# Kernel optimization log

Hardware: AMD Instinct MI355X
Metric: run time of the kernel (lower is better)

Reference implementation:

```python
import jax, jax.numpy as jnp
import numpy as np

N_GRAPHS = 1000  # static number of segments for mean pooling
NUM_STEPS = 6


def setup_inputs() -> dict:
    key = jax.random.key(0)
    ks = jax.random.split(key, 20)
    N, E, G = 100000, 1600000, N_GRAPHS
    H, FN, FE = 64, 9, 3

    def init(k, shape, fan_in):
        return (jax.random.normal(k, shape) / np.sqrt(fan_in)).astype(jnp.float32)

    return {
        "x": jax.random.normal(ks[0], (N, FN), dtype=jnp.float32),
        "edge_index": jax.random.randint(ks[1], (2, E), 0, N, dtype=jnp.int32),
        "edge_attr": jax.random.normal(ks[2], (E, FE), dtype=jnp.float32),
        "batch": jnp.sort(jax.random.randint(ks[3], (N,), 0, G, dtype=jnp.int32)),
        # message MLP: Linear(FN+FE -> H), ReLU, Linear(H -> H)
        "msg_W1": init(ks[4], (H, FN + FE), FN + FE), "msg_b1": jnp.zeros((H,), jnp.float32),
        "msg_W2": init(ks[5], (H, H), H), "msg_b2": jnp.zeros((H,), jnp.float32),
        # GRUCell(H, H): torch layout weight_ih [3H, H], weight_hh [3H, H]
        "gru_Wih": init(ks[6], (3 * H, H), H), "gru_Whh": init(ks[7], (3 * H, H), H),
        "gru_bih": jnp.zeros((3 * H,), jnp.float32), "gru_bhh": jnp.zeros((3 * H,), jnp.float32),
        # readout: Linear(H -> H), ReLU, Dropout(eval: identity), Linear(H -> 1)
        "read_W1": init(ks[8], (H, H), H), "read_b1": jnp.zeros((H,), jnp.float32),
        "read_W2": init(ks[9], (1, H), H), "read_b2": jnp.zeros((1,), jnp.float32),
    }


def reference(x, edge_index, edge_attr, batch,
              msg_W1, msg_b1, msg_W2, msg_b2,
              gru_Wih, gru_Whh, gru_bih, gru_bhh,
              read_W1, read_b1, read_W2, read_b2):
    N = x.shape[0]
    H = msg_W2.shape[0]
    src, dst = edge_index[0], edge_index[1]

    # Messages depend only on x[src] and edge_attr, which never change across
    # steps, so (identically to the torch loop) compute them once.
    m_in = jnp.concatenate([x[src], edge_attr], axis=1)          # [E, FN+FE]
    h1 = jax.nn.relu(m_in @ msg_W1.T + msg_b1)                    # [E, H]
    messages = h1 @ msg_W2.T + msg_b2                             # [E, H]
    aggregated = jax.ops.segment_sum(messages, dst, num_segments=N)  # [N, H]

    # GRU input-gate projections of `aggregated` are also step-invariant.
    gi = aggregated @ gru_Wih.T + gru_bih                          # [N, 3H]
    i_r, i_z, i_n = jnp.split(gi, 3, axis=1)

    h = jnp.zeros((N, H), dtype=x.dtype)
    for _ in range(NUM_STEPS):
        gh = h @ gru_Whh.T + gru_bhh                               # [N, 3H]
        h_r, h_z, h_n = jnp.split(gh, 3, axis=1)
        r = jax.nn.sigmoid(i_r + h_r)
        z = jax.nn.sigmoid(i_z + h_z)
        n = jnp.tanh(i_n + r * h_n)
        h = (1.0 - z) * n + z * h

    # global_mean_pool
    sums = jax.ops.segment_sum(h, batch, num_segments=N_GRAPHS)    # [G, H]
    counts = jax.ops.segment_sum(jnp.ones((N,), h.dtype), batch, num_segments=N_GRAPHS)
    pooled = sums / jnp.maximum(counts, 1.0)[:, None]

    out = jax.nn.relu(pooled @ read_W1.T + read_b1)                # dropout=eval identity
    return out @ read_W2.T + read_b2                               # [G, 1]
```

## Files before the change

kernel.cpp:

```cpp
#include <hip/hip_runtime.h>
#include <math.h>

#define CH 1024
#define LOG2E 1.4426950408889634f

typedef __attribute__((ext_vector_type(8))) short bf16x8;
typedef __attribute__((ext_vector_type(4))) float f32x4;
typedef __attribute__((ext_vector_type(4))) unsigned u32x4;

__device__ __forceinline__ float rcp_(float x){ return __builtin_amdgcn_rcpf(x); }
__device__ __forceinline__ float exp2_(float x){ return exp2f(x); }
__device__ __forceinline__ unsigned short f2bf(float f){
  union{float f;unsigned u;}v; v.f=f;
  unsigned r = v.u + 0x7fffu + ((v.u>>16)&1u);
  return (unsigned short)(r>>16);
}
__device__ __forceinline__ float bf2f(unsigned short u){
  union{unsigned u; float f;} v; v.u = ((unsigned)u) << 16; return v.f;
}

__global__ __launch_bounds__(256) void count_rank(const int* __restrict__ ei, int* __restrict__ cnt,
                                                  int* __restrict__ rank, int E){
  int e = blockIdx.x*256 + threadIdx.x;
  if (e < E) rank[e] = atomicAdd(&cnt[ei[E + e]], 1);
}

__global__ __launch_bounds__(256) void scan_partial(const int* __restrict__ cnt, int* __restrict__ bsum, int N){
  __shared__ int s[256];
  int b = blockIdx.x, t = threadIdx.x;
  int base = b*CH;
  int sum = 0;
  for (int i = t; i < CH; i += 256){ int idx = base + i; sum += (idx < N) ? cnt[idx] : 0; }
  s[t] = sum; __syncthreads();
  for (int off = 128; off > 0; off >>= 1){ if (t < off) s[t] += s[t+off]; __syncthreads(); }
  if (t == 0) bsum[b] = s[0];
}

__global__ void scan_bsum(int* __restrict__ bsum, int B){
  if (threadIdx.x == 0 && blockIdx.x == 0){
    int acc = 0;
    for (int i = 0; i < B; i++){ int v = bsum[i]; bsum[i] = acc; acc += v; }
  }
}

__global__ __launch_bounds__(256) void scan_final(const int* __restrict__ cnt, const int* __restrict__ bsum,
                                                  int* __restrict__ off, float* __restrict__ degf, int N, int E){
  __shared__ int s[256];
  __shared__ int sx[256];
  int b = blockIdx.x, t = threadIdx.x;
  int i0 = b*CH + t*4;
  int v0 = (i0   < N) ? cnt[i0]   : 0;
  int v1 = (i0+1 < N) ? cnt[i0+1] : 0;
  int v2 = (i0+2 < N) ? cnt[i0+2] : 0;
  int v3 = (i0+3 < N) ? cnt[i0+3] : 0;
  s[t] = v0+v1+v2+v3; __syncthreads();
  if (t == 0){ int acc = bsum[b]; for (int i = 0; i < 256; i++){ sx[i] = acc; acc += s[i]; } }
  __syncthreads();
  int acc = sx[t];
  if (i0   < N){ off[i0]   = acc; degf[i0]   = (float)v0; } acc += v0;
  if (i0+1 < N){ off[i0+1] = acc; degf[i0+1] = (float)v1; } acc += v1;
  if (i0+2 < N){ off[i0+2] = acc; degf[i0+2] = (float)v2; } acc += v2;
  if (i0+3 < N){ off[i0+3] = acc; degf[i0+3] = (float)v3; }
  if (b == 0 && t == 0) off[N] = E;
}

__global__ __launch_bounds__(256) void xpack_kernel(const float* __restrict__ x, unsigned short* __restrict__ xp, int N){
  int n = blockIdx.x*256 + threadIdx.x;
  if (n >= N) return;
  const float* xr = x + (size_t)n*9;
  union { unsigned short us[32]; u32x4 q[4]; } row;
  #pragma unroll
  for (int i = 0; i < 9; i++){
    unsigned short hi = f2bf(xr[i]);
    unsigned short lo = f2bf(xr[i] - bf2f(hi));
    if (i < 8){ row.us[i] = hi; row.us[8+i] = lo; }
    else { row.us[16] = hi; row.us[17] = lo; }
  }
  #pragma unroll
  for (int i = 18; i < 32; i++) row.us[i] = 0;
  u32x4* dstp = (u32x4*)(xp + (size_t)n*32);
  dstp[0] = row.q[0]; dstp[1] = row.q[1]; dstp[2] = row.q[2]; dstp[3] = row.q[3];
}

__global__ __launch_bounds__(256) void fill64(const int* __restrict__ ei, const unsigned short* __restrict__ xp,
                                              const float* __restrict__ ea, const int* __restrict__ off,
                                              const int* __restrict__ rank, float* __restrict__ csr2, int E){
  int e = blockIdx.x*256 + threadIdx.x;
  if (e >= E) return;
  int dst = ei[E + e];
  int src = ei[e];
  int p = off[dst] + rank[e];
  const u32x4* xr4 = (const u32x4*)(xp + (size_t)src*32);
  u32x4 q0 = xr4[0];
  u32x4 q1 = xr4[1];
  unsigned hl8 = *(const unsigned*)(xp + (size_t)src*32 + 16);
  const float* er = ea + (size_t)e*3;
  float e0 = er[0], e1 = er[1], e2 = er[2];
  unsigned short eh0 = f2bf(e0), eh1 = f2bf(e1), eh2 = f2bf(e2);
  unsigned short el0 = f2bf(e0 - bf2f(eh0));
  unsigned short el1 = f2bf(e1 - bf2f(eh1));
  unsigned short el2 = f2bf(e2 - bf2f(eh2));
  u32x4 q2;
  q2.x = (hl8 & 0xFFFFu) | ((unsigned)eh0 << 16);
  q2.y = (unsigned)eh1 | ((unsigned)eh2 << 16);
  q2.z = (hl8 >> 16)    | ((unsigned)el0 << 16);
  q2.w = (unsigned)el1 | ((unsigned)el2 << 16);
  u32x4 q3 = {0u, 0u, 0u, 0u};
  u32x4* row = (u32x4*)(csr2 + (size_t)p*16);
  row[0] = q0; row[1] = q1; row[2] = q2; row[3] = q3;
}

__global__ __launch_bounds__(256) void pack_frag(const float* __restrict__ W, unsigned short* __restrict__ P,
                                                 float sRZ, float sN){
  int o = blockIdx.x*256 + threadIdx.x;
  if (o >= 12288) return;
  int j = o & 7, l = (o>>3)&63, kh = (o>>9)&1, c = o>>10;
  float sc = (c < 8) ? sRZ : sN;
  P[o] = f2bf(sc * W[(c*16 + (l&15))*64 + kh*32 + 8*(l>>4) + j]);
}

__global__ __launch_bounds__(256) void pack_w1(const float* __restrict__ W1,
    unsigned short* __restrict__ B1, unsigned short* __restrict__ B2){
  int o = blockIdx.x*256 + threadIdx.x;
  if (o >= 2048) return;
  int j = o & 7, l = (o>>3) & 63, c = o >> 9;
  int n = c*16 + (l & 15);
  int kk = 8*(l>>4) + j;
  unsigned short b1v = 0, b2v = 0;
  if (kk < 12){
    float w = W1[n*12 + kk];
    unsigned short hi = f2bf(w);
    b1v = hi;
    b2v = f2bf(w - bf2f(hi));
  } else if (kk >= 16 && kk < 28){
    b1v = f2bf(W1[n*12 + (kk-16)]);
  }
  B1[o] = b1v; B2[o] = b2v;
}

__global__ __launch_bounds__(256) void make_M(const float* __restrict__ Wih, const float* __restrict__ W2,
    const float* __restrict__ b2, float* __restrict__ M, float* __restrict__ dv){
  int idx = blockIdx.x*256 + threadIdx.x;
  if (idx >= 12288) return;
  int o = idx >> 6, k = idx & 63;
  float sc = (o < 128) ? -LOG2E : 2.0f*LOG2E;
  float acc = 0.0f;
  for (int j = 0; j < 64; j++) acc += Wih[o*64+j]*W2[j*64+k];
  M[idx] = sc * acc;
  if (k == 0){
    float a2 = 0.0f;
    for (int j = 0; j < 64; j++) a2 += Wih[o*64+j]*b2[j];
    dv[o] = sc * a2;
  }
}

__global__ __launch_bounds__(256, 2) void node_msg_kernel(
    const float* __restrict__ csr2, const int* __restrict__ off,
    const unsigned short* __restrict__ W1B1v, const unsigned short* __restrict__ W1B2v,
    const float* __restrict__ b1, float* __restrict__ hsum, int N)
{
  int t = threadIdx.x, lane = t & 63;
  int s_ = lane & 15, g_ = lane >> 4;
  const bf16x8* B1 = (const bf16x8*)W1B1v;
  const bf16x8* B2 = (const bf16x8*)W1B2v;
  bf16x8 w1b1[4], w1b2[4];
  #pragma unroll
  for (int c = 0; c < 4; c++){ w1b1[c] = B1[c*64+lane]; w1b2[c] = B2[c*64+lane]; }
  float b1f[4], rb1[4];
  #pragma unroll
  for (int c = 0; c < 4; c++){ b1f[c] = b1[c*16+s_]; rb1[c] = fmaxf(b1f[c], 0.f); }
  bool hi_ = (g_ < 2);
  int rofs_us = (g_ == 0) ? 0 : (g_ == 2) ? 8 : (g_ == 1) ? 16 : 20;
  int wid = (blockIdx.x*256 + t) >> 6;
  int nw = gridDim.x*4;
  for (int node = wid; node < N; node += nw){
    int s = off[node], e = off[node+1];
    float accR[4] = {0.f,0.f,0.f,0.f};
    int ntiles = (e - s + 15) >> 4;
    for (int tt = 0; tt < ntiles; tt++){
      int p = s + tt*16 + s_;
      bf16x8 af = {0,0,0,0,0,0,0,0};
      if (p < e){
        const unsigned short* row = (const unsigned short*)(csr2 + (size_t)p*16);
        if ((g_ & 1) == 0){
          af = *(const bf16x8*)(row + rofs_us);
        } else {
          short4 v = *(const short4*)(row + rofs_us);
          af[0]=v.x; af[1]=v.y; af[2]=v.z; af[3]=v.w;
        }
      }
      bf16x8 ah = hi_ ? af : (bf16x8){0,0,0,0,0,0,0,0};
      #pragma unroll
      for (int c = 0; c < 4; c++){
        f32x4 acc; acc[0]=b1f[c]; acc[1]=b1f[c]; acc[2]=b1f[c]; acc[3]=b1f[c];
        acc = __builtin_amdgcn_mfma_f32_16x16x32_bf16(af, w1b1[c], acc, 0,0,0);
        acc = __builtin_amdgcn_mfma_f32_16x16x32_bf16(ah, w1b2[c], acc, 0,0,0);
        accR[c] += fmaxf(acc[0],0.f)+fmaxf(acc[1],0.f)+fmaxf(acc[2],0.f)+fmaxf(acc[3],0.f);
      }
    }
    float npad = (float)(ntiles*16 - (e - s));
    #pragma unroll
    for (int c = 0; c < 4; c++){
      float v = accR[c] - npad*rb1[c];
      v += __shfl_xor(v, 16, 64);
      v += __shfl_xor(v, 32, 64);
      accR[c] = v;
    }
    float outv = (g_==0) ? accR[0] : ((g_==1) ? accR[1] : ((g_==2) ? accR[2] : accR[3]));
    hsum[(size_t)node*64 + lane] = outv;
  }
}

__global__ __launch_bounds__(256, 2) void gru_mfma(
    float* hsumh,
    const unsigned short* __restrict__ MF, const unsigned short* __restrict__ WhhF,
    const float* __restrict__ bih, const float* __restrict__ bhh,
    const float* __restrict__ dv, const float* __restrict__ degf, int N)
{
  __shared__ __align__(16) unsigned short swhh[12288];
  __shared__ unsigned short hbuf[4][1024];
  __shared__ float sbi[192], sbh[192], sdv[192];
  int t = threadIdx.x, lane = t & 63, w = t >> 6;
  int s_ = lane & 15, g_ = lane >> 4;
  unsigned short* hb = hbuf[w];

  {
    const u32x4* src = (const u32x4*)WhhF;
    u32x4* dst = (u32x4*)swhh;
    #pragma unroll
    for (int i = 0; i < 6; i++) dst[t + 256*i] = src[t + 256*i];
  }
  if (t < 192){ sbi[t] = bih[t]; sbh[t] = bhh[t]; sdv[t] = dv[t]; }
  __syncthreads();

  const bf16x8* WHH = (const bf16x8*)swhh;
  const bf16x8* MFV = (const bf16x8*)MF;

  float bhn[4];
  #pragma unroll
  for (int c = 0; c < 4; c++) bhn[c] = 2.0f*LOG2E * sbh[128 + c*16 + s_];

  int NT = (N + 15) >> 4;
  int wid = blockIdx.x*4 + w;
  int nw = gridDim.x*4;
  for (int tile = wid; tile < NT; tile += nw){
    int nodeA = tile*16 + s_; if (nodeA > N-1) nodeA = N-1;
    const float* ab = hsumh + (size_t)nodeA*64 + g_*8;
    float4 v0 = *(const float4*)(ab);
    float4 v1 = *(const float4*)(ab+4);
    float4 v2 = *(const float4*)(ab+32);
    float4 v3 = *(const float4*)(ab+36);
    bf16x8 a0, a1;
    a0[0]=(short)f2bf(v0.x); a0[1]=(short)f2bf(v0.y); a0[2]=(short)f2bf(v0.z); a0[3]=(short)f2bf(v0.w);
    a0[4]=(short)f2bf(v1.x); a0[5]=(short)f2bf(v1.y); a0[6]=(short)f2bf(v1.z); a0[7]=(short)f2bf(v1.w);
    a1[0]=(short)f2bf(v2.x); a1[1]=(short)f2bf(v2.y); a1[2]=(short)f2bf(v2.z); a1[3]=(short)f2bf(v2.w);
    a1[4]=(short)f2bf(v3.x); a1[5]=(short)f2bf(v3.y); a1[6]=(short)f2bf(v3.z); a1[7]=(short)f2bf(v3.w);

    float4 dr = *(const float4*)(degf + tile*16 + 4*g_);
    float drr[4] = {dr.x, dr.y, dr.z, dr.w};
    bf16x8 gb[6];
    #pragma unroll
    for (int c = 0; c < 12; c++){
      float sc = (c < 8) ? -LOG2E : 2.0f*LOG2E;
      float bic = sc * (sbi[c*16 + s_] + ((c < 8) ? sbh[c*16 + s_] : 0.0f));
      float dvc = sdv[c*16 + s_];
      f32x4 acc;
      #pragma unroll
      for (int r = 0; r < 4; r++) acc[r] = bic + drr[r]*dvc;
      acc = __builtin_amdgcn_mfma_f32_16x16x32_bf16(a0, MFV[(c*2+0)*64 + lane], acc, 0, 0, 0);
      acc = __builtin_amdgcn_mfma_f32_16x16x32_bf16(a1, MFV[(c*2+1)*64 + lane], acc, 0, 0, 0);
      #pragma unroll
      for (int r = 0; r < 4; r++) gb[c>>1][(c&1)*4 + r] = (short)f2bf(acc[r]);
    }

    f32x4 hD[4];
    #pragma unroll
    for (int c = 0; c < 4; c++){ hD[c][0]=0.f; hD[c][1]=0.f; hD[c][2]=0.f; hD[c][3]=0.f; }
    bf16x8 h0 = {0,0,0,0,0,0,0,0};
    bf16x8 h1 = {0,0,0,0,0,0,0,0};
    for (int st = 0; st < 6; st++){
      int zofs = 0;
      asm volatile("" : "+v"(zofs));
      #pragma unroll
      for (int c = 0; c < 4; c++){
        f32x4 aR, aZ, aN, giN;
        #pragma unroll
        for (int r = 0; r < 4; r++){
          aR[r]  = bf2f((unsigned short)gb[c>>1][(c&1)*4 + r]);
          aZ[r]  = bf2f((unsigned short)gb[(4+c)>>1][((4+c)&1)*4 + r]);
          giN[r] = bf2f((unsigned short)gb[(8+c)>>1][((8+c)&1)*4 + r]);
        }
        aN[0]=bhn[c]; aN[1]=bhn[c]; aN[2]=bhn[c]; aN[3]=bhn[c];
        aR = __builtin_amdgcn_mfma_f32_16x16x32_bf16(h0, WHH[(c*2)*64 + lane + zofs],       aR, 0,0,0);
        aR = __builtin_amdgcn_mfma_f32_16x16x32_bf16(h1, WHH[(c*2+1)*64 + lane + zofs],     aR, 0,0,0);
        aZ = __builtin_amdgcn_mfma_f32_16x16x32_bf16(h0, WHH[((4+c)*2)*64 + lane + zofs],   aZ, 0,0,0);
        aZ = __builtin_amdgcn_mfma_f32_16x16x32_bf16(h1, WHH[((4+c)*2+1)*64 + lane + zofs], aZ, 0,0,0);
        aN = __builtin_amdgcn_mfma_f32_16x16x32_bf16(h0, WHH[((8+c)*2)*64 + lane + zofs],   aN, 0,0,0);
        aN = __builtin_amdgcn_mfma_f32_16x16x32_bf16(h1, WHH[((8+c)*2+1)*64 + lane + zofs], aN, 0,0,0);
        #pragma unroll
        for (int r = 0; r < 4; r++){
          float rr = rcp_(1.0f + exp2_(aR[r]));
          float zz = rcp_(1.0f + exp2_(aZ[r]));
          float nn = 1.0f - 2.0f*rcp_(1.0f + exp2_(giN[r] + rr*aN[r]));
          hD[c][r] = nn + zz*(hD[c][r] - nn);
        }
      }
      if (st < 5){
        #pragma unroll
        for (int c = 0; c < 4; c++){
          #pragma unroll
          for (int r = 0; r < 4; r++){
            int nl = 4*g_ + r;
            int idx = (nl*64 + 16*c + s_) ^ ((nl & 7) << 3);
            hb[idx] = f2bf(hD[c][r]);
          }
        }
        int r0 = (s_*64 +      8*g_) ^ ((s_ & 7) << 3);
        int r1 = (s_*64 + 32 + 8*g_) ^ ((s_ & 7) << 3);
        h0 = *(const bf16x8*)(hb + r0);
        h1 = *(const bf16x8*)(hb + r1);
      }
    }
    #pragma unroll
    for (int c = 0; c < 4; c++){
      #pragma unroll
      for (int r = 0; r < 4; r++){
        int node = tile*16 + 4*g_ + r;
        if (node < N) hsumh[(size_t)node*64 + 16*c + s_] = hD[c][r];
      }
    }
  }
}

__global__ __launch_bounds__(256) void gstart_kernel(const int* __restrict__ batch, int* __restrict__ gstart, int N, int G){
  int g = blockIdx.x*256 + threadIdx.x;
  if (g > G) return;
  int lo = 0, hi = N;
  while (lo < hi){ int mid = (lo + hi) >> 1; if (batch[mid] < g) lo = mid + 1; else hi = mid; }
  gstart[g] = lo;
}

__global__ __launch_bounds__(64) void pool_kernel(const float* __restrict__ hout, const int* __restrict__ gstart,
                                                  float* __restrict__ pooled, int G){
  int g = blockIdx.x; int lane = threadIdx.x;
  int s = gstart[g], e = gstart[g+1];
  float acc = 0.0f;
  for (int n = s; n < e; n++) acc += hout[(size_t)n*64 + lane];
  float c = fmaxf((float)(e - s), 1.0f);
  pooled[g*64 + lane] = acc / c;
}

__global__ __launch_bounds__(256) void readout_kernel(
  const float* __restrict__ pooled,
  const float* __restrict__ W1, const float* __restrict__ b1,
  const float* __restrict__ W2, const float* __restrict__ b2,
  float* __restrict__ out, int G)
{
  __shared__ __align__(16) float sW1[64*64];
  __shared__ float sb1[64], sW2v[64];
  for (int i = threadIdx.x; i < 64*64; i += 256) sW1[i] = W1[i];
  if (threadIdx.x < 64){ sb1[threadIdx.x] = b1[threadIdx.x]; sW2v[threadIdx.x] = W2[threadIdx.x]; }
  __syncthreads();
  int g = blockIdx.x*256 + threadIdx.x;
  if (g >= G) return;
  float p[64];
  const float4* pp = (const float4*)(pooled + g*64);
  #pragma unroll
  for (int k4 = 0; k4 < 16; k4++){
    float4 v = pp[k4];
    p[4*k4] = v.x; p[4*k4+1] = v.y; p[4*k4+2] = v.z; p[4*k4+3] = v.w;
  }
  float acc = b2[0];
  for (int j = 0; j < 64; j++){
    const float4* wv4 = (const float4*)(sW1 + j*64);
    float tacc = sb1[j];
    #pragma unroll
    for (int k4 = 0; k4 < 16; k4++){
      float4 wv = wv4[k4];
      tacc += wv.x*p[4*k4] + wv.y*p[4*k4+1] + wv.z*p[4*k4+2] + wv.w*p[4*k4+3];
    }
    acc += sW2v[j]*fmaxf(tacc, 0.0f);
  }
  out[g] = acc;
}

extern "C" void kernel_launch(void* const* d_in, const int* in_sizes, int n_in,
                              void* d_out, int out_size, void* d_ws, size_t ws_size,
                              hipStream_t stream)
{
  const float* x    = (const float*)d_in[0];
  const int*   ei   = (const int*)  d_in[1];
  const float* ea   = (const float*)d_in[2];
  const int*   batch= (const int*)  d_in[3];
  const float* mW1  = (const float*)d_in[4];
  const float* mb1  = (const float*)d_in[5];
  const float* mW2  = (const float*)d_in[6];
  const float* mb2  = (const float*)d_in[7];
  const float* Wih  = (const float*)d_in[8];
  const float* Whh  = (const float*)d_in[9];
  const float* bih  = (const float*)d_in[10];
  const float* bhh  = (const float*)d_in[11];
  const float* rW1  = (const float*)d_in[12];
  const float* rb1  = (const float*)d_in[13];
  const float* rW2  = (const float*)d_in[14];
  const float* rb2  = (const float*)d_in[15];
  float* out = (float*)d_out;

  int N = in_sizes[0] / 9;
  int E = in_sizes[1] / 2;
  int G = out_size;

  float* fws    = (float*)d_ws;
  float* hsum   = fws;
  int*   rank   = (int*)hsum;
  float* csr2   = hsum + (size_t)64*N;
  float* degf   = csr2 + (size_t)16*E;
  float* M      = degf + (size_t)(N+16);
  float* dv     = M + 12288;
  float* pooled = dv + 192;
  unsigned short* MF   = (unsigned short*)(pooled + (size_t)64*G);
  unsigned short* WhhF = MF + 12288;
  unsigned short* W1B1 = WhhF + 12288;
  unsigned short* W1B2 = W1B1 + 2048;
  unsigned short* xp   = W1B2 + 2048;
  int*   iws    = (int*)(xp + (size_t)32*N);
  int*   cnt    = iws;
  int*   off    = cnt + N;
  int*   bsum   = off + N + 1;
  int*   gstart = bsum + 1024;

  int B1 = (N + CH - 1) / CH;

  hipMemsetAsync(cnt, 0, (size_t)N*sizeof(int), stream);
  hipMemsetAsync(degf + N, 0, 16*sizeof(float), stream);

  count_rank<<<(E+255)/256, 256, 0, stream>>>(ei, cnt, rank, E);
  scan_partial<<<B1, 256, 0, stream>>>(cnt, bsum, N);
  scan_bsum<<<1, 64, 0, stream>>>(bsum, B1);
  scan_final<<<B1, 256, 0, stream>>>(cnt, bsum, off, degf, N, E);
  xpack_kernel<<<(N+255)/256, 256, 0, stream>>>(x, xp, N);
  fill64<<<(E+255)/256, 256, 0, stream>>>(ei, xp, ea, off, rank, csr2, E);

  pack_w1<<<8, 256, 0, stream>>>(mW1, W1B1, W1B2);
  make_M<<<48, 256, 0, stream>>>(Wih, mW2, mb2, M, dv);
  pack_frag<<<48, 256, 0, stream>>>(M, MF, 1.0f, 1.0f);
  pack_frag<<<48, 256, 0, stream>>>(Whh, WhhF, -LOG2E, 2.0f*LOG2E);

  node_msg_kernel<<<1024, 256, 0, stream>>>(csr2, off, W1B1, W1B2, mb1, hsum, N);

  gru_mfma<<<1024, 256, 0, stream>>>(hsum, MF, WhhF, bih, bhh, dv, degf, N);

  gstart_kernel<<<(G+256)/256, 256, 0, stream>>>(batch, gstart, N, G);
  pool_kernel<<<G, 64, 0, stream>>>(hsum, gstart, pooled, G);
  readout_kernel<<<(G+255)/256, 256, 0, stream>>>(pooled, rW1, rb1, rW2, rb2, out, G);
}
```

Before: 332.9 us.

## Replace per-edge 64-byte CSR rows with 16-byte records and gather node features

New measurement: 322.0 us, median of 2. -3.3%, faster.

```diff
diff --git a/kernel.cpp b/kernel.cpp
--- a/kernel.cpp
+++ b/kernel.cpp
@@ -82,32 +82,26 @@
   dstp[0] = row.q[0]; dstp[1] = row.q[1]; dstp[2] = row.q[2]; dstp[3] = row.q[3];
 }
 
-__global__ __launch_bounds__(256) void fill64(const int* __restrict__ ei, const unsigned short* __restrict__ xp,
-                                              const float* __restrict__ ea, const int* __restrict__ off,
-                                              const int* __restrict__ rank, float* __restrict__ csr2, int E){
+__global__ __launch_bounds__(256) void fill_rec(const int* __restrict__ ei, const float* __restrict__ ea,
+                                                const int* __restrict__ off, const int* __restrict__ rank,
+                                                u32x4* __restrict__ rec, int E){
   int e = blockIdx.x*256 + threadIdx.x;
   if (e >= E) return;
   int dst = ei[E + e];
   int src = ei[e];
   int p = off[dst] + rank[e];
-  const u32x4* xr4 = (const u32x4*)(xp + (size_t)src*32);
-  u32x4 q0 = xr4[0];
-  u32x4 q1 = xr4[1];
-  unsigned hl8 = *(const unsigned*)(xp + (size_t)src*32 + 16);
   const float* er = ea + (size_t)e*3;
   float e0 = er[0], e1 = er[1], e2 = er[2];
   unsigned short eh0 = f2bf(e0), eh1 = f2bf(e1), eh2 = f2bf(e2);
   unsigned short el0 = f2bf(e0 - bf2f(eh0));
   unsigned short el1 = f2bf(e1 - bf2f(eh1));
   unsigned short el2 = f2bf(e2 - bf2f(eh2));
-  u32x4 q2;
-  q2.x = (hl8 & 0xFFFFu) | ((unsigned)eh0 << 16);
-  q2.y = (unsigned)eh1 | ((unsigned)eh2 << 16);
-  q2.z = (hl8 >> 16)    | ((unsigned)el0 << 16);
-  q2.w = (unsigned)el1 | ((unsigned)el2 << 16);
-  u32x4 q3 = {0u, 0u, 0u, 0u};
-  u32x4* row = (u32x4*)(csr2 + (size_t)p*16);
-  row[0] = q0; row[1] = q1; row[2] = q2; row[3] = q3;
+  u32x4 r;
+  r.x = (unsigned)src;
+  r.y = (unsigned)eh0 | ((unsigned)eh1 << 16);
+  r.z = (unsigned)eh2 | ((unsigned)el0 << 16);
+  r.w = (unsigned)el1 | ((unsigned)el2 << 16);
+  rec[p] = r;
 }
 
 __global__ __launch_bounds__(256) void pack_frag(const float* __restrict__ W, unsigned short* __restrict__ P,
@@ -155,7 +149,7 @@
 }
 
 __global__ __launch_bounds__(256, 2) void node_msg_kernel(
-    const float* __restrict__ csr2, const int* __restrict__ off,
+    const u32x4* __restrict__ rec, const unsigned short* __restrict__ xp, const int* __restrict__ off,
     const unsigned short* __restrict__ W1B1v, const unsigned short* __restrict__ W1B2v,
     const float* __restrict__ b1, float* __restrict__ hsum, int N)
 {
@@ -170,7 +164,6 @@
   #pragma unroll
   for (int c = 0; c < 4; c++){ b1f[c] = b1[c*16+s_]; rb1[c] = fmaxf(b1f[c], 0.f); }
   bool hi_ = (g_ < 2);
-  int rofs_us = (g_ == 0) ? 0 : (g_ == 2) ? 8 : (g_ == 1) ? 16 : 20;
   int wid = (blockIdx.x*256 + t) >> 6;
   int nw = gridDim.x*4;
   for (int node = wid; node < N; node += nw){
@@ -181,12 +174,24 @@
       int p = s + tt*16 + s_;
       bf16x8 af = {0,0,0,0,0,0,0,0};
       if (p < e){
-        const unsigned short* row = (const unsigned short*)(csr2 + (size_t)p*16);
+        u32x4 r = rec[p];
+        int src = (int)r.x;
+        const unsigned short* xr = xp + (size_t)src*32;
         if ((g_ & 1) == 0){
-          af = *(const bf16x8*)(row + rofs_us);
+          af = *(const bf16x8*)(xr + ((g_ == 0) ? 0 : 8));
         } else {
-          short4 v = *(const short4*)(row + rofs_us);
-          af[0]=v.x; af[1]=v.y; af[2]=v.z; af[3]=v.w;
+          unsigned hl8 = *(const unsigned*)(xr + 16);
+          if (g_ == 1){
+            af[0] = (short)(hl8 & 0xFFFFu);
+            af[1] = (short)(r.y & 0xFFFFu);
+            af[2] = (short)(r.y >> 16);
+            af[3] = (short)(r.z & 0xFFFFu);
+          } else {
+            af[0] = (short)(hl8 >> 16);
+            af[1] = (short)(r.z >> 16);
+            af[2] = (short)(r.w & 0xFFFFu);
+            af[3] = (short)(r.w >> 16);
+          }
         }
       }
       bf16x8 ah = hi_ ? af : (bf16x8){0,0,0,0,0,0,0,0};
@@ -413,8 +418,8 @@
   float* fws    = (float*)d_ws;
   float* hsum   = fws;
   int*   rank   = (int*)hsum;
-  float* csr2   = hsum + (size_t)64*N;
-  float* degf   = csr2 + (size_t)16*E;
+  float* recf   = hsum + (size_t)64*N;
+  float* degf   = recf + (size_t)4*E;
   float* M      = degf + (size_t)(N+16);
   float* dv     = M + 12288;
   float* pooled = dv + 192;
@@ -428,6 +433,7 @@
   int*   off    = cnt + N;
   int*   bsum   = off + N + 1;
   int*   gstart = bsum + 1024;
+  u32x4* rec    = (u32x4*)recf;
 
   int B1 = (N + CH - 1) / CH;
 
@@ -439,14 +445,14 @@
   scan_bsum<<<1, 64, 0, stream>>>(bsum, B1);
   scan_final<<<B1, 256, 0, stream>>>(cnt, bsum, off, degf, N, E);
   xpack_kernel<<<(N+255)/256, 256, 0, stream>>>(x, xp, N);
-  fill64<<<(E+255)/256, 256, 0, stream>>>(ei, xp, ea, off, rank, csr2, E);
+  fill_rec<<<(E+255)/256, 256, 0, stream>>>(ei, ea, off, rank, rec, E);
 
   pack_w1<<<8, 256, 0, stream>>>(mW1, W1B1, W1B2);
   make_M<<<48, 256, 0, stream>>>(Wih, mW2, mb2, M, dv);
   pack_frag<<<48, 256, 0, stream>>>(M, MF, 1.0f, 1.0f);
   pack_frag<<<48, 256, 0, stream>>>(Whh, WhhF, -LOG2E, 2.0f*LOG2E);
 
-  node_msg_kernel<<<1024, 256, 0, stream>>>(csr2, off, W1B1, W1B2, mb1, hsum, N);
+  node_msg_kernel<<<1024, 256, 0, stream>>>(rec, xp, off, W1B1, W1B2, mb1, hsum, N);
 
   gru_mfma<<<1024, 256, 0, stream>>>(hsum, MF, WhhF, bih, bhh, dv, degf, N);
 
```
